# Kernel tuning notes

Hardware: AMD Instinct MI355X
Metric: run time of the kernel (lower is better)

Reference implementation:

```python
import jax, jax.numpy as jnp
import numpy as np

D_MODEL = 512
KERNEL = 16
DILATIONS = (1, 1, 2, 2, 4, 4, 8, 8)
HEADS = len(DILATIONS)
HEAD_W = D_MODEL // HEADS
B, L = 2, 1024
MODE = "forward"  # causal: window sees only prior words


def setup_inputs() -> dict:
    key = jax.random.key(0)
    ks = jax.random.split(key, 8)
    s = 0.02  # small init like nn.Linear
    return {
        "tensor": jax.random.normal(ks[0], (B, L, D_MODEL), jnp.float32),
        "Wq": jax.random.normal(ks[1], (HEADS, HEAD_W, D_MODEL), jnp.float32) * s,
        "bq": jnp.zeros((HEADS, HEAD_W), jnp.float32),
        "Wk": jax.random.normal(ks[2], (HEADS, KERNEL, HEAD_W, D_MODEL), jnp.float32) * s,
        "bk": jnp.zeros((HEADS, KERNEL, HEAD_W), jnp.float32),
        "Wv": jax.random.normal(ks[3], (HEADS, KERNEL, HEAD_W, D_MODEL), jnp.float32) * s,
        "bv": jnp.zeros((HEADS, KERNEL, HEAD_W), jnp.float32),
        "Wo": jax.random.normal(ks[4], (D_MODEL, HEADS, HEAD_W), jnp.float32) * s,
        "bo": jnp.zeros((D_MODEL,), jnp.float32),
    }


def _window_indices():
    """Static gather indices replicating Glimpses.dilocal's dilated unfold.

    Returns idx of shape (H, L, K) indexing into a sequence zero-padded by
    max_off on both sides: content[h, l, k] = x_padded[idx[h, l, k]].
    """
    dil = np.asarray(DILATIONS)  # (H,)
    max_off = int((KERNEL - 1) * dil.max())
    if MODE == "forward":
        front = (KERNEL - 1) * dil           # all padding in front (causal)
    elif MODE == "backward":
        front = np.zeros_like(dil)           # all padding behind
    else:  # center
        front = ((KERNEL - 1) * dil) // 2
    l = np.arange(L)[None, :, None]
    k = np.arange(KERNEL)[None, None, :]
    d = dil[:, None, None]
    f = front[:, None, None]
    idx = l + k * d - f + max_off            # (H, L, K), always in-range
    return jnp.asarray(idx), max_off


_IDX, _MOFF = _window_indices()


def reference(tensor, Wq, bq, Wk, bk, Wv, bv, Wo, bo):
    # tensor: (B, L, D)
    xp = jnp.pad(tensor, ((0, 0), (_MOFF, _MOFF), (0, 0)))
    content = xp[:, _IDX, :]                                   # (B,H,L,K,D)
    # per-head query projection (kernel position 1)
    q = jnp.einsum('bld,hod->bhlo', tensor, Wq) + bq[:, None, :]        # (B,H,L,hw)
    # per-(head, kernel-position) independent key/value projections
    k = jnp.einsum('bhlkd,hkod->bhlko', content, Wk) + bk[:, None, :, :]
    v = jnp.einsum('bhlkd,hkod->bhlko', content, Wv) + bv[:, None, :, :]
    # tiny local attention over the K window positions
    logits = jnp.einsum('bhlo,bhlko->bhlk', q, k)               # (B,H,L,K)
    score = jax.nn.softmax(logits, axis=-1)
    # NOTE: original scales AFTER the score@value matmul (faithful to source)
    attn = jnp.einsum('bhlk,bhlko->bhlo', score, v)
    attn = attn / jnp.sqrt(jnp.asarray(HEAD_W, tensor.dtype))   # (B,H,L,hw)
    # dehead: merge (heads, head_width) -> d_model
    out = jnp.einsum('bhlo,dho->bld', attn, Wo) + bo            # (B,L,D)
    return out
```

## Files before the change

### kernel.cpp

```cpp
#include <hip/hip_runtime.h>


#define BD 2
#define LL 1024
#define DM 512
#define HH 8
#define KT 16
#define HW 64

#define NQKV 16896

typedef unsigned short u16;
typedef unsigned int u32;
typedef __bf16 bf16x8 __attribute__((ext_vector_type(8)));
typedef float f32x4 __attribute__((ext_vector_type(4)));
typedef unsigned short ushort4v __attribute__((ext_vector_type(4)));
typedef unsigned short ushort8v __attribute__((ext_vector_type(8)));

__constant__ int c_dil[8] = {1, 1, 2, 2, 4, 4, 8, 8};

__device__ __forceinline__ float bf2f(u16 u) {
    return __builtin_bit_cast(float, (u32)u << 16);
}
__device__ __forceinline__ u16 f2bf(float f) {
    u32 u = __builtin_bit_cast(u32, f);
    return (u16)((u + 0x7fffu + ((u >> 16) & 1u)) >> 16);
}

__device__ __forceinline__ void gl_lds16(const u16* g, u16* l) {
    __builtin_amdgcn_global_load_lds(
        (__attribute__((address_space(1))) void*)g,
        (__attribute__((address_space(3))) void*)l, 16, 0, 0);
}

__global__ __launch_bounds__(256, 4) void gemm_bf16(
    const u16* __restrict__ A, const u16* __restrict__ Bm,
    const float* __restrict__ bq, const float* __restrict__ bk,
    const float* __restrict__ bv,
    u16* __restrict__ qb, u16* __restrict__ kvb)
{
    const int bid = blockIdx.x;
    const int wg  = (bid & 7) * 264 + (bid >> 3);
    const int m0  = (wg & 15) << 7;
    const int n0  = (wg >> 4) << 7;

    __shared__ u16 As[2][128 * 32];
    __shared__ u16 Bs[2][128 * 32];

    const int tid  = threadIdx.x;
    const int wave = tid >> 6, lane = tid & 63;
    const int r0 = tid >> 2;
    const int cc = (tid & 3) << 3;
    const int mw = (wave >> 1) << 6;
    const int nw = (wave & 1) << 6;
    const int lr = lane & 15;
    const int qg = lane >> 4;
    const int ksw = ((qg ^ ((lr >> 1) & 3)) << 3);

    const u16* Ag = A  + (size_t)(m0 + r0) * DM + cc;
    const u16* Bg = Bm + (size_t)(n0 + r0) * DM + cc;
    u16* lA = &As[0][0] + tid * 8;
    u16* lB = &Bs[0][0] + tid * 8;

#define STG(ko, c) do {                                                    \
        gl_lds16(Ag + (ko),                  lA + (c) * 4096);             \
        gl_lds16(Ag + (ko) + (size_t)64*DM,  lA + (c) * 4096 + 2048);      \
        gl_lds16(Bg + (ko),                  lB + (c) * 4096);             \
        gl_lds16(Bg + (ko) + (size_t)64*DM,  lB + (c) * 4096 + 2048);      \
    } while (0)

    f32x4 acc[4][4];
#pragma unroll
    for (int i = 0; i < 4; ++i)
#pragma unroll
        for (int j = 0; j < 4; ++j) acc[i][j] = (f32x4){0.f, 0.f, 0.f, 0.f};

    STG(0, 0);
    __syncthreads();

#pragma unroll
    for (int kc = 0; kc < 16; ++kc) {
        const int cur = kc & 1;
        if (kc < 15) STG((kc + 1) << 5, cur ^ 1);

        bf16x8 af[4], bfr[4];
#pragma unroll
        for (int i = 0; i < 4; ++i)
            af[i] = *(const bf16x8*)&As[cur][(mw + (i << 4) + lr) * 32 + ksw];
#pragma unroll
        for (int j = 0; j < 4; ++j)
            bfr[j] = *(const bf16x8*)&Bs[cur][(nw + (j << 4) + lr) * 32 + ksw];
#pragma unroll
        for (int i = 0; i < 4; ++i)
#pragma unroll
            for (int j = 0; j < 4; ++j)
                acc[i][j] = __builtin_amdgcn_mfma_f32_16x16x32_bf16(
                    af[i], bfr[j], acc[i][j], 0, 0, 0);

        __syncthreads();
    }
#undef STG

    if (n0 < 512) {
#pragma unroll
        for (int i = 0; i < 4; ++i) {
            const int rowb = m0 + mw + (i << 4) + (qg << 2);
#pragma unroll
            for (int j = 0; j < 4; ++j) {
                const int col = n0 + nw + (j << 4) + lr;
                const float bs = bq[col];
#pragma unroll
                for (int r = 0; r < 4; ++r)
                    qb[(size_t)(rowb + r) * 512 + col] =
                        f2bf(acc[i][j][r] + bs);
            }
        }
    } else {
        const int reg = (n0 >= 8704);
        const float* bias = reg ? bv : bk;
        const int t0  = n0 - (reg ? 8704 : 512);
        const int h   = t0 >> 10;
        const int pb  = ((reg << 3) + h) << 4;
#pragma unroll
        for (int i = 0; i < 4; ++i) {
            const int rowb = m0 + mw + (i << 4) + (qg << 2);
#pragma unroll
            for (int j = 0; j < 4; ++j) {
                const int tcol  = (t0 & 1023) + nw + (j << 4) + lr;
                const int kslot = tcol >> 6;
                const int oo    = tcol & 63;
                const float bs  = bias[(h << 10) + tcol];
#pragma unroll
                for (int r = 0; r < 4; ++r) {
                    const int row = rowb + r;
                    const int bb  = row >> 10, l2 = row & 1023;
                    kvb[((size_t)(((pb + kslot) << 1) + bb) << 16)
                        + (l2 << 6) + oo] = f2bf(acc[i][j][r] + bs);
                }
            }
        }
    }
}

__global__ __launch_bounds__(256, 4) void gemm_out(
    const u16* __restrict__ A, const u16* __restrict__ Bm,
    const float* __restrict__ bias, float* __restrict__ C)
{
    __shared__ u16 As[2][64 * 32];
    __shared__ u16 Bs[2][64 * 32];

    const int tid  = threadIdx.x;
    const int wave = tid >> 6, lane = tid & 63;
    const int m0 = blockIdx.y << 6, n0 = blockIdx.x << 6;
    const int r0 = tid >> 2, cc = (tid & 3) << 3;
    const int mw = wave << 4;
    const int lr = lane & 15, qg = lane >> 4;
    const int ksw = ((qg ^ ((lr >> 1) & 3)) << 3);

    const u16* Ag = A  + (size_t)(m0 + r0) * DM + cc;
    const u16* Bg = Bm + (size_t)(n0 + r0) * DM + cc;
    u16* lA = &As[0][0] + tid * 8;
    u16* lB = &Bs[0][0] + tid * 8;

#define STG(ko, c) do {                                                    \
        gl_lds16(Ag + (ko), lA + (c) * 2048);                              \
        gl_lds16(Bg + (ko), lB + (c) * 2048);                              \
    } while (0)

    f32x4 acc[4];
#pragma unroll
    for (int j = 0; j < 4; ++j) acc[j] = (f32x4){0.f, 0.f, 0.f, 0.f};

    STG(0, 0);
    __syncthreads();

#pragma unroll
    for (int kc = 0; kc < 16; ++kc) {
        const int cur = kc & 1;
        if (kc < 15) STG((kc + 1) << 5, cur ^ 1);

        bf16x8 af = *(const bf16x8*)&As[cur][(mw + lr) * 32 + ksw];
#pragma unroll
        for (int j = 0; j < 4; ++j) {
            bf16x8 bfr = *(const bf16x8*)&Bs[cur][((j << 4) + lr) * 32 + ksw];
            acc[j] = __builtin_amdgcn_mfma_f32_16x16x32_bf16(af, bfr, acc[j], 0, 0, 0);
        }
        __syncthreads();
    }
#undef STG

#pragma unroll
    for (int j = 0; j < 4; ++j) {
        const int col = n0 + (j << 4) + lr;
        const float bs = bias[col];
#pragma unroll
        for (int r = 0; r < 4; ++r)
            C[(size_t)(m0 + mw + (qg << 2) + r) * DM + col] = acc[j][r] + bs;
    }
}

__global__ void cvt_swz(const float* __restrict__ x,  const float* __restrict__ Wq,
                        const float* __restrict__ Wk, const float* __restrict__ Wv,
                        const float* __restrict__ Wo,
                        u16* __restrict__ xb, u16* __restrict__ wb,
                        u16* __restrict__ wob)
{
    const int i = blockIdx.x * 256 + threadIdx.x;
    const float* src; u16* dst; int t;
    if (i < 131072) {
        t = i;
        src = x;  dst = xb;
    } else if (i < 1212416) {
        t = i - 131072;
        const int row = t >> 6;
        if      (row <  512) src = Wq;
        else if (row < 8704) src = Wk - (size_t)512 * DM;
        else                 src = Wv - (size_t)8704 * DM;
        dst = wb;
    } else {
        t = i - 1212416;
        src = Wo; dst = wob;
    }
    const int row = t >> 6;
    const int c8  = t & 63;
    const int s   = (row >> 1) & 3;
    const int oc  = (c8 & ~3) | ((c8 & 3) ^ s);
    const float* p = src + (size_t)row * DM + (oc << 3);
    float4 v0 = *(const float4*)p;
    float4 v1 = *(const float4*)(p + 4);
    ushort8v o = { f2bf(v0.x), f2bf(v0.y), f2bf(v0.z), f2bf(v0.w),
                   f2bf(v1.x), f2bf(v1.y), f2bf(v1.z), f2bf(v1.w) };
    *(ushort8v*)(dst + (size_t)row * DM + (c8 << 3)) = o;
}

__global__ __launch_bounds__(256, 4) void attn_bf16(
    const u16* __restrict__ qb,
    const u16* __restrict__ kvb,
    const float* __restrict__ bk,
    const float* __restrict__ bv,
    u16* __restrict__ attnb)
{
    const int tid = threadIdx.x;
    const int j  = tid & 7;
    const int ll = tid >> 3;
    const int bid = blockIdx.x;
    const int h = bid & 7;
    const int t = (bid >> 3) & 31;
    const int b = bid >> 8;
    const int l = (t << 5) + ll;
    const int dil = c_dil[h];

    const int hko = h * (KT * HW);

    float qf[8];
    {
        ushort8v qv = *(const ushort8v*)(qb + (size_t)(b * LL + l) * 512
                                         + h * HW + (j << 3));
#pragma unroll
        for (int z = 0; z < 8; ++z) qf[z] = bf2f(qv[z]);
    }

    const u16* kbase = kvb + ((size_t)(((h << 4) << 1) + b) << 16) + (j << 3);
    const u16* vbase = kbase + ((size_t)(8 << 4) << 17);

    ushort8v kr[KT];
#pragma unroll
    for (int k = 0; k < KT; ++k) {
        const int src = l - (KT - 1 - k) * dil;
        if (src >= 0)
            kr[k] = *(const ushort8v*)(kbase + ((size_t)k << 17) + (src << 6));
    }

    float lg[KT];
#pragma unroll
    for (int k = 0; k < KT; ++k) {
        const int src = l - (KT - 1 - k) * dil;
        float p = 0.f;
        if (src >= 0) {
#pragma unroll
            for (int z = 0; z < 8; ++z) p += qf[z] * bf2f(kr[k][z]);
        } else {
            const float* bkp = bk + hko + k * HW + (j << 3);
#pragma unroll
            for (int z = 0; z < 8; ++z) p += qf[z] * bkp[z];
        }
        p += __shfl_xor(p, 1);
        p += __shfl_xor(p, 2);
        p += __shfl_xor(p, 4);
        lg[k] = p;
    }

    float m = lg[0];
#pragma unroll
    for (int k = 1; k < KT; ++k) m = fmaxf(m, lg[k]);
    float s = 0.f;
#pragma unroll
    for (int k = 0; k < KT; ++k) { lg[k] = __expf(lg[k] - m); s += lg[k]; }
    const float inv = 1.f / s;

    ushort8v vr[KT];
#pragma unroll
    for (int k = 0; k < KT; ++k) {
        const int src = l - (KT - 1 - k) * dil;
        if (src >= 0)
            vr[k] = *(const ushort8v*)(vbase + ((size_t)k << 17) + (src << 6));
    }

    float acc[8];
#pragma unroll
    for (int z = 0; z < 8; ++z) acc[z] = 0.f;
#pragma unroll
    for (int k = 0; k < KT; ++k) {
        const int src = l - (KT - 1 - k) * dil;
        const float sc = lg[k] * inv;
        if (src >= 0) {
#pragma unroll
            for (int z = 0; z < 8; ++z) acc[z] = fmaf(sc, bf2f(vr[k][z]), acc[z]);
        } else {
            const float* bvp = bv + hko + k * HW + (j << 3);
#pragma unroll
            for (int z = 0; z < 8; ++z) acc[z] = fmaf(sc, bvp[z], acc[z]);
        }
    }

    ushort8v o;
#pragma unroll
    for (int z = 0; z < 8; ++z) o[z] = f2bf(acc[z] * 0.125f);
    const int row = b * LL + l;
    const int k8 = h * 8 + j;
    const int sw = ((k8 & 3) ^ ((l >> 1) & 3)) << 3;
    *(ushort8v*)(attnb + (size_t)row * DM + ((k8 >> 2) << 5) + sw) = o;
}

__global__ __launch_bounds__(256, 2) void gemm_nt_bias(
    const float* __restrict__ A, const float* __restrict__ Bm,
    const float* __restrict__ bias, float* __restrict__ C,
    int M, int N, int Kd)
{
    __shared__ float As[16][68];
    __shared__ float Bs[16][68];
    const int tid = threadIdx.x;
    const int tx = tid & 15, ty = tid >> 4;
    const int r0 = blockIdx.y << 6, c0 = blockIdx.x << 6;
    const int lr = tid >> 2, k4 = (tid & 3) << 2;
    const float* Ap = A  + (size_t)(r0 + lr) * Kd + k4;
    const float* Bp = Bm + (size_t)(c0 + lr) * Kd + k4;
    float acc[4][4];
#pragma unroll
    for (int i = 0; i < 4; ++i)
#pragma unroll
        for (int j = 0; j < 4; ++j) acc[i][j] = 0.f;
    for (int d0 = 0; d0 < Kd; d0 += 16) {
        float4 av = *(const float4*)(Ap + d0);
        float4 bv = *(const float4*)(Bp + d0);
        As[k4 + 0][lr] = av.x; As[k4 + 1][lr] = av.y;
        As[k4 + 2][lr] = av.z; As[k4 + 3][lr] = av.w;
        Bs[k4 + 0][lr] = bv.x; Bs[k4 + 1][lr] = bv.y;
        Bs[k4 + 2][lr] = bv.z; Bs[k4 + 3][lr] = bv.w;
        __syncthreads();
#pragma unroll
        for (int dd = 0; dd < 16; ++dd) {
            float4 a4 = *(const float4*)&As[dd][ty << 2];
            float4 b4 = *(const float4*)&Bs[dd][tx << 2];
            float ar[4] = {a4.x, a4.y, a4.z, a4.w};
            float br[4] = {b4.x, b4.y, b4.z, b4.w};
#pragma unroll
            for (int i = 0; i < 4; ++i)
#pragma unroll
                for (int j = 0; j < 4; ++j)
                    acc[i][j] = fmaf(ar[i], br[j], acc[i][j]);
        }
        __syncthreads();
    }
#pragma unroll
    for (int i = 0; i < 4; ++i) {
        float4 o;
        const int c = c0 + (tx << 2);
        o.x = acc[i][0] + bias[c + 0];
        o.y = acc[i][1] + bias[c + 1];
        o.z = acc[i][2] + bias[c + 2];
        o.w = acc[i][3] + bias[c + 3];
        *(float4*)&C[(size_t)(r0 + (ty << 2) + i) * N + c] = o;
    }
}

__device__ __forceinline__ void tile_gemm_f32(
    const float* __restrict__ xb, int src, bool ok,
    const float* __restrict__ wrow,
    int lr, int k4, int tx, int ty,
    float (&As)[16][68], float (&Ws)[16][68], float (&acc)[4][4])
{
#pragma unroll
    for (int i = 0; i < 4; ++i)
#pragma unroll
        for (int j = 0; j < 4; ++j) acc[i][j] = 0.f;
    const float* xrow = xb + (size_t)(ok ? src : 0) * DM + k4;
    for (int d0 = 0; d0 < DM; d0 += 16) {
        float4 av = make_float4(0.f, 0.f, 0.f, 0.f);
        if (ok) av = *(const float4*)(xrow + d0);
        float4 wv = *(const float4*)(wrow + d0);
        As[k4 + 0][lr] = av.x; As[k4 + 1][lr] = av.y;
        As[k4 + 2][lr] = av.z; As[k4 + 3][lr] = av.w;
        Ws[k4 + 0][lr] = wv.x; Ws[k4 + 1][lr] = wv.y;
        Ws[k4 + 2][lr] = wv.z; Ws[k4 + 3][lr] = wv.w;
        __syncthreads();
#pragma unroll
        for (int dd = 0; dd < 16; ++dd) {
            float4 a4 = *(const float4*)&As[dd][ty << 2];
            float4 b4 = *(const float4*)&Ws[dd][tx << 2];
            float ar[4] = {a4.x, a4.y, a4.z, a4.w};
            float br[4] = {b4.x, b4.y, b4.z, b4.w};
#pragma unroll
            for (int i = 0; i < 4; ++i)
#pragma unroll
                for (int j = 0; j < 4; ++j)
                    acc[i][j] = fmaf(ar[i], br[j], acc[i][j]);
        }
        __syncthreads();
    }
}

__global__ __launch_bounds__(256, 2) void attn_kernel(
    const float* __restrict__ x, const float* __restrict__ q,
    const float* __restrict__ Wk, const float* __restrict__ bk,
    const float* __restrict__ Wv, const float* __restrict__ bv,
    float* __restrict__ attn)
{
    __shared__ float As[16][68];
    __shared__ float Ws[16][68];
    __shared__ float qs[64][68];
    __shared__ float lg[64][17];
    __shared__ float red[64][17];
    const int tid = threadIdx.x;
    const int tx = tid & 15, ty = tid >> 4;
    const int bid = blockIdx.x;
    const int h = bid & 7, t = (bid >> 3) & 15, b = bid >> 7;
    const int l0 = t << 6;
    const int dil = c_dil[h];
    const int lr = tid >> 2, k4 = (tid & 3) << 2;
    for (int i = tid; i < 64 * 16; i += 256) {
        int l = i >> 4, o4 = (i & 15) << 2;
        float4 v = *(const float4*)&q[((size_t)(b * LL + l0 + l) * HH + h) * HW + o4];
        *(float4*)&qs[l][o4] = v;
    }
    const float* xb  = x  + (size_t)b * LL * DM;
    const float* Wkh = Wk + (size_t)h * KT * HW * DM;
    const float* Wvh = Wv + (size_t)h * KT * HW * DM;
    const float* bkh = bk + h * KT * HW;
    const float* bvh = bv + h * KT * HW;
    float acc[4][4];
    for (int kk = 0; kk < KT; ++kk) {
        const int src = l0 + lr - (KT - 1 - kk) * dil;
        const bool ok = (src >= 0) && (src < LL);
        tile_gemm_f32(xb, src, ok, Wkh + (size_t)(kk * HW + lr) * DM + k4,
                      lr, k4, tx, ty, As, Ws, acc);
        const float* bkp = bkh + kk * HW + (tx << 2);
#pragma unroll
        for (int i = 0; i < 4; ++i) {
            float p = 0.f;
#pragma unroll
            for (int j = 0; j < 4; ++j)
                p += (acc[i][j] + bkp[j]) * qs[(ty << 2) + i][(tx << 2) + j];
            red[(ty << 2) + i][tx] = p;
        }
        __syncthreads();
        if (tid < 64) {
            float s = 0.f;
#pragma unroll
            for (int u = 0; u < 16; ++u) s += red[tid][u];
            lg[tid][kk] = s;
        }
        __syncthreads();
    }
    if (tid < 64) {
        float m = lg[tid][0];
#pragma unroll
        for (int u = 1; u < KT; ++u) m = fmaxf(m, lg[tid][u]);
        float s = 0.f;
#pragma unroll
        for (int u = 0; u < KT; ++u) {
            float e = expf(lg[tid][u] - m);
            lg[tid][u] = e; s += e;
        }
        float inv = 1.f / s;
#pragma unroll
        for (int u = 0; u < KT; ++u) lg[tid][u] *= inv;
    }
    __syncthreads();
    float vacc[4][4];
#pragma unroll
    for (int i = 0; i < 4; ++i)
#pragma unroll
        for (int j = 0; j < 4; ++j) vacc[i][j] = 0.f;
    for (int kk = 0; kk < KT; ++kk) {
        const int src = l0 + lr - (KT - 1 - kk) * dil;
        const bool ok = (src >= 0) && (src < LL);
        tile_gemm_f32(xb, src, ok, Wvh + (size_t)(kk * HW + lr) * DM + k4,
                      lr, k4, tx, ty, As, Ws, acc);
        const float* bvp = bvh + kk * HW + (tx << 2);
#pragma unroll
        for (int i = 0; i < 4; ++i) {
            float sc = lg[(ty << 2) + i][kk];
#pragma unroll
            for (int j = 0; j < 4; ++j)
                vacc[i][j] = fmaf(sc, acc[i][j] + bvp[j], vacc[i][j]);
        }
    }
#pragma unroll
    for (int i = 0; i < 4; ++i) {
        float4 o;
        o.x = vacc[i][0] * 0.125f;
        o.y = vacc[i][1] * 0.125f;
        o.z = vacc[i][2] * 0.125f;
        o.w = vacc[i][3] * 0.125f;
        *(float4*)&attn[((size_t)(b * LL + l0 + (ty << 2) + i) * HH + h) * HW + (tx << 2)] = o;
    }
}

extern "C" void kernel_launch(void* const* d_in, const int* in_sizes, int n_in,
                              void* d_out, int out_size, void* d_ws, size_t ws_size,
                              hipStream_t stream)
{
    const float* x  = (const float*)d_in[0];
    const float* Wq = (const float*)d_in[1];
    const float* bq = (const float*)d_in[2];
    const float* Wk = (const float*)d_in[3];
    const float* bk = (const float*)d_in[4];
    const float* Wv = (const float*)d_in[5];
    const float* bv = (const float*)d_in[6];
    const float* Wo = (const float*)d_in[7];
    const float* bo = (const float*)d_in[8];
    float* out = (float*)d_out;

    const int M = BD * LL;

    const size_t N_X   = (size_t)BD * LL * DM;
    const size_t N_WB  = (size_t)NQKV * DM;
    const size_t N_WO  = (size_t)DM * DM;
    const size_t N_QKV = (size_t)M * NQKV;
    const size_t NEED  = (N_X + N_WB + N_WO + N_QKV + N_X) * 2;

    if (ws_size >= NEED) {
        u16* xb    = (u16*)d_ws;
        u16* wb    = xb    + N_X;
        u16* wob   = wb    + N_WB;
        u16* qb    = wob   + N_WO;
        u16* kvb   = qb    + N_X;
        u16* attnb = qb    + N_QKV;

        cvt_swz<<<4864, 256, 0, stream>>>(x, Wq, Wk, Wv, Wo, xb, wb, wob);

        gemm_bf16<<<dim3(2112), 256, 0, stream>>>(
            xb, wb, bq, bk, bv, qb, kvb);

        attn_bf16<<<BD * HH * (LL / 32), 256, 0, stream>>>(
            qb, kvb, bk, bv, attnb);

        gemm_out<<<dim3(8, 32), 256, 0, stream>>>(attnb, wob, bo, out);
    } else {
        float* qws = (float*)d_ws;
        float* aws = qws + (size_t)BD * LL * HH * HW;
        gemm_nt_bias<<<dim3((HH * HW) / 64, M / 64), 256, 0, stream>>>(
            x, Wq, bq, qws, M, HH * HW, DM);
        attn_kernel<<<BD * HH * (LL / 64), 256, 0, stream>>>(
            x, qws, Wk, bk, Wv, bv, aws);
        gemm_nt_bias<<<dim3(DM / 64, M / 64), 256, 0, stream>>>(
            aws, Wo, bo, out, M, DM, HH * HW);
    }
}
```

Baseline: 171.9 us.

## Triple-buffer LDS staging with explicit vmcnt waits in both GEMMs

Both GEMM kernels move from double to triple buffering of A/B tiles in LDS. Two tiles are prefetched ahead, and the full __syncthreads is replaced by an explicit s_waitcnt vmcnt on the outstanding global-to-LDS loads plus a raw s_barrier, so the newest prefetch stays in flight across the barrier. The goal is to hide global load latency better. In exchange, LDS per block grows, and the main GEMM's launch bound drops from 4 to 3 blocks per SM, which may reduce occupancy.

```diff
diff --git a/kernel.cpp b/kernel.cpp
--- a/kernel.cpp
+++ b/kernel.cpp
@@ -33,7 +33,13 @@
         (__attribute__((address_space(3))) void*)l, 16, 0, 0);
 }
 
-__global__ __launch_bounds__(256, 4) void gemm_bf16(
+__device__ __forceinline__ void bar() {
+    asm volatile("" ::: "memory");
+    __builtin_amdgcn_s_barrier();
+    asm volatile("" ::: "memory");
+}
+
+__global__ __launch_bounds__(256, 3) void gemm_bf16(
     const u16* __restrict__ A, const u16* __restrict__ Bm,
     const float* __restrict__ bq, const float* __restrict__ bk,
     const float* __restrict__ bv,
@@ -44,8 +50,8 @@
     const int m0  = (wg & 15) << 7;
     const int n0  = (wg >> 4) << 7;
 
-    __shared__ u16 As[2][128 * 32];
-    __shared__ u16 Bs[2][128 * 32];
+    __shared__ u16 As[3][128 * 32];
+    __shared__ u16 Bs[3][128 * 32];
 
     const int tid  = threadIdx.x;
     const int wave = tid >> 6, lane = tid & 63;
@@ -62,11 +68,12 @@
     u16* lA = &As[0][0] + tid * 8;
     u16* lB = &Bs[0][0] + tid * 8;
 
-#define STG(ko, c) do {                                                    \
-        gl_lds16(Ag + (ko),                  lA + (c) * 4096);             \
-        gl_lds16(Ag + (ko) + (size_t)64*DM,  lA + (c) * 4096 + 2048);      \
-        gl_lds16(Bg + (ko),                  lB + (c) * 4096);             \
-        gl_lds16(Bg + (ko) + (size_t)64*DM,  lB + (c) * 4096 + 2048);      \
+#define STG(t2, c) do {                                                    \
+        const int ko_ = (t2) << 5;                                         \
+        gl_lds16(Ag + ko_,                  lA + (c) * 4096);              \
+        gl_lds16(Ag + ko_ + (size_t)64*DM,  lA + (c) * 4096 + 2048);       \
+        gl_lds16(Bg + ko_,                  lB + (c) * 4096);              \
+        gl_lds16(Bg + ko_ + (size_t)64*DM,  lB + (c) * 4096 + 2048);       \
     } while (0)
 
     f32x4 acc[4][4];
@@ -76,12 +83,14 @@
         for (int j = 0; j < 4; ++j) acc[i][j] = (f32x4){0.f, 0.f, 0.f, 0.f};
 
     STG(0, 0);
-    __syncthreads();
-
-#pragma unroll
-    for (int kc = 0; kc < 16; ++kc) {
-        const int cur = kc & 1;
-        if (kc < 15) STG((kc + 1) << 5, cur ^ 1);
+    STG(1, 1);
+    asm volatile("s_waitcnt vmcnt(4)" ::: "memory");
+    bar();
+
+#pragma unroll
+    for (int t = 0; t < 16; ++t) {
+        const int cur = t % 3;
+        if (t < 14) STG(t + 2, (t + 2) % 3);
 
         bf16x8 af[4], bfr[4];
 #pragma unroll
@@ -97,7 +106,11 @@
                 acc[i][j] = __builtin_amdgcn_mfma_f32_16x16x32_bf16(
                     af[i], bfr[j], acc[i][j], 0, 0, 0);
 
-        __syncthreads();
+        if (t < 14)
+            asm volatile("s_waitcnt vmcnt(4)" ::: "memory");
+        else if (t == 14)
+            asm volatile("s_waitcnt vmcnt(0)" ::: "memory");
+        if (t < 15) bar();
     }
 #undef STG
 
@@ -146,8 +159,8 @@
     const u16* __restrict__ A, const u16* __restrict__ Bm,
     const float* __restrict__ bias, float* __restrict__ C)
 {
-    __shared__ u16 As[2][64 * 32];
-    __shared__ u16 Bs[2][64 * 32];
+    __shared__ u16 As[3][64 * 32];
+    __shared__ u16 Bs[3][64 * 32];
 
     const int tid  = threadIdx.x;
     const int wave = tid >> 6, lane = tid & 63;
@@ -162,9 +175,10 @@
     u16* lA = &As[0][0] + tid * 8;
     u16* lB = &Bs[0][0] + tid * 8;
 
-#define STG(ko, c) do {                                                    \
-        gl_lds16(Ag + (ko), lA + (c) * 2048);                              \
-        gl_lds16(Bg + (ko), lB + (c) * 2048);                              \
+#define STG(t2, c) do {                                                    \
+        const int ko_ = (t2) << 5;                                         \
+        gl_lds16(Ag + ko_, lA + (c) * 2048);                               \
+        gl_lds16(Bg + ko_, lB + (c) * 2048);                               \
     } while (0)
 
     f32x4 acc[4];
@@ -172,12 +186,14 @@
     for (int j = 0; j < 4; ++j) acc[j] = (f32x4){0.f, 0.f, 0.f, 0.f};
 
     STG(0, 0);
-    __syncthreads();
-
-#pragma unroll
-    for (int kc = 0; kc < 16; ++kc) {
-        const int cur = kc & 1;
-        if (kc < 15) STG((kc + 1) << 5, cur ^ 1);
+    STG(1, 1);
+    asm volatile("s_waitcnt vmcnt(2)" ::: "memory");
+    bar();
+
+#pragma unroll
+    for (int t = 0; t < 16; ++t) {
+        const int cur = t % 3;
+        if (t < 14) STG(t + 2, (t + 2) % 3);
 
         bf16x8 af = *(const bf16x8*)&As[cur][(mw + lr) * 32 + ksw];
 #pragma unroll
@@ -185,7 +201,12 @@
             bf16x8 bfr = *(const bf16x8*)&Bs[cur][((j << 4) + lr) * 32 + ksw];
             acc[j] = __builtin_amdgcn_mfma_f32_16x16x32_bf16(af, bfr, acc[j], 0, 0, 0);
         }
-        __syncthreads();
+
+        if (t < 14)
+            asm volatile("s_waitcnt vmcnt(2)" ::: "memory");
+        else if (t == 14)
+            asm volatile("s_waitcnt vmcnt(0)" ::: "memory");
+        if (t < 15) bar();
     }
 #undef STG
 
```

After: 168.8 us. Within noise of the previous version (-1.8%).
